# Kernel tuning notes

Measured on AMD Instinct MI355X. Metric: run time of the kernel, lower is better.

## Reference

```python
import jax, jax.numpy as jnp
import numpy as np

D_MODEL = 512
NUM_HEADS = 8
WINDOW = 10
DEPTH = D_MODEL // NUM_HEADS


def positional_encoding(position, d_model):
    pos = np.arange(position)[:, None].astype(np.float32)
    i = np.arange(d_model)[None, :].astype(np.float32)
    angle = pos / np.power(10000.0, 2.0 * (np.floor(i / 2.0)) / np.float32(d_model))
    angle[:, 0::2] = np.sin(angle[:, 0::2])
    angle[:, 1::2] = np.cos(angle[:, 1::2])
    return jnp.asarray(angle[None, ...], dtype=jnp.float32)  # [1, n, d_model]


def forward(x, wq_w, wq_b, wk_w, wk_b, wv_w, wv_b, dense_w, dense_b):
    B, C, S, _ = x.shape
    data = x[..., 0]
    mask = x[..., 2]
    data = data.reshape(B, C, -1, WINDOW)   # [B,C,n,W]
    mask = mask.reshape(B, C, -1, WINDOW)
    n = data.shape[2]

    # mean_module: (data*mask).mean over window, drop first/last window
    mean_feature = jnp.mean(data * mask, axis=-1, keepdims=True)[:, :, 1:-1]  # [B,C,n-2,1]

    # combined look-ahead + padding mask
    mask_min = jnp.min(mask[:, :, 1:-1], axis=-1)              # [B,C,n-2]
    n2 = n - 2
    look_ahead = 1.0 - jnp.tril(jnp.ones((n2, n2), jnp.float32))
    padding = (mask_min == 0).astype(jnp.float32)[:, :, None, None, :]  # [B,C,1,1,n-2]
    comb_mask = jnp.maximum(look_ahead, padding)               # [B,C,1,n-2,n-2]

    # positional encoding over window dimension
    pe = positional_encoding(n, WINDOW)                        # [1,n,W]
    data = data + pe[None]                                     # [B,C,n,W]

    # q,k from concatenated future/past windows; v from current windows
    qk_in = jnp.concatenate([data[:, :, 2:], data[:, :, :-2]], axis=-1)  # [B,C,n-2,2W]
    q = qk_in @ wq_w + wq_b
    k = qk_in @ wk_w + wk_b
    v = data[:, :, 1:-1] @ wv_w + wv_b                          # [B,C,n-2,d_model]

    def split_heads(t):
        return t.reshape(B, C, n2, NUM_HEADS, DEPTH).transpose(0, 1, 3, 2, 4)

    q, k, v = split_heads(q), split_heads(k), split_heads(v)    # [B,C,H,n-2,depth]

    logits = jnp.einsum('bchqd,bchkd->bchqk', q, k) / jnp.sqrt(jnp.float32(DEPTH))
    logits = logits + comb_mask * (-1e9)
    attn = jax.nn.softmax(logits, axis=-1)
    ctx = jnp.einsum('bchqk,bchkd->bchqd', attn, v)
    ctx = ctx.transpose(0, 1, 3, 2, 4).reshape(B, C, n2, D_MODEL)

    concat = jnp.concatenate([ctx, mean_feature], axis=-1)      # [B,C,n-2,d_model+1]
    out = concat @ dense_w + dense_b                            # [B,C,n-2,W]
    return out.reshape(B, C, -1)[..., None]                     # [B,C,(n-2)*W,1]


def setup_inputs() -> dict:
    key = jax.random.key(0)
    ks = jax.random.split(key, 8)
    B, C, S = 16, 16, 2560
    data = jax.random.normal(ks[0], (B, C, S), jnp.float32)
    time = jnp.zeros((B, C, S), jnp.float32)
    mask = (jax.random.uniform(ks[1], (B, C, S)) < 0.9).astype(jnp.float32)
    x = jnp.stack([data, time, mask], axis=-1)
    scale = 0.02
    return {
        'x': x,
        'wq_w': jax.random.normal(ks[2], (2 * WINDOW, D_MODEL), jnp.float32) * scale,
        'wq_b': jnp.zeros((D_MODEL,), jnp.float32),
        'wk_w': jax.random.normal(ks[3], (2 * WINDOW, D_MODEL), jnp.float32) * scale,
        'wk_b': jnp.zeros((D_MODEL,), jnp.float32),
        'wv_w': jax.random.normal(ks[4], (WINDOW, D_MODEL), jnp.float32) * scale,
        'wv_b': jnp.zeros((D_MODEL,), jnp.float32),
        'dense_w': jax.random.normal(ks[5], (D_MODEL + 1, WINDOW), jnp.float32) * scale,
        'dense_b': jnp.zeros((WINDOW,), jnp.float32),
    }


def reference(x, wq_w, wq_b, wk_w, wk_b, wv_w, wv_b, dense_w, dense_b):
    return forward(x, wq_w, wq_b, wk_w, wk_b, wv_w, wv_b, dense_w, dense_b)
```

## Files before the change

kernel.cpp:

```cpp
#include <hip/hip_runtime.h>

#define LOG2E 1.44269504088896340736f

typedef __bf16 bf16x8 __attribute__((ext_vector_type(8)));
typedef float f32x16 __attribute__((ext_vector_type(16)));

union U4B { uint4 u; bf16x8 v; };

static __device__ __forceinline__ unsigned short f2bf(float f) {
  unsigned u = __builtin_bit_cast(unsigned, f);
  u += 0x7FFFu + ((u >> 16) & 1u);
  return (unsigned short)(u >> 16);
}
static __device__ __forceinline__ float bf2f(unsigned short s) {
  unsigned u = ((unsigned)s) << 16;
  return __builtin_bit_cast(float, u);
}
static __device__ __forceinline__ f32x16 zero16() {
  f32x16 z;
#pragma unroll
  for (int i = 0; i < 16; ++i) z[i] = 0.f;
  return z;
}
static __device__ __forceinline__ f32x16 MFMA(bf16x8 a, bf16x8 b, f32x16 c) {
  return __builtin_amdgcn_mfma_f32_32x32x16_bf16(a, b, c, 0, 0, 0);
}

static __device__ __forceinline__ void xform(f32x16 t, int hi, uint4& f0, uint4& f1) {
  unsigned pk[8], sw[8];
#pragma unroll
  for (int s = 0; s < 8; ++s) {
    unsigned d;
    asm("v_cvt_pk_bf16_f32 %0, %1, %2" : "=v"(d) : "v"(t[2*s]), "v"(t[2*s+1]));
    pk[s] = d;
  }
#pragma unroll
  for (int s = 0; s < 8; ++s) sw[s] = (unsigned)__shfl_xor((int)pk[s], 32);
  if (hi) {
    f0 = make_uint4(sw[2], sw[3], pk[2], pk[3]);
    f1 = make_uint4(sw[6], sw[7], pk[6], pk[7]);
  } else {
    f0 = make_uint4(pk[0], pk[1], sw[0], sw[1]);
    f1 = make_uint4(pk[4], pk[5], sw[4], sw[5]);
  }
}

__global__ void zero_out_k(float* __restrict__ out, int n) {
  int i = blockIdx.x * 256 + threadIdx.x;
  if (i < n) out[i] = 0.f;
}

__global__ void setup_k(
    const float* __restrict__ wq_w, const float* __restrict__ wq_b,
    const float* __restrict__ wk_w, const float* __restrict__ wk_b,
    const float* __restrict__ wv_w, const float* __restrict__ wv_b,
    const float* __restrict__ dense_w, float* __restrict__ ws)
{
  int gid = blockIdx.x*256 + threadIdx.x;
  float* pe = ws;
  unsigned short* wqT = (unsigned short*)(ws + 2560);
  unsigned short* wkT = (unsigned short*)(ws + 10752);
  float* WVD = ws + 18944;
  float* bvd = ws + 19744;
  if (gid < 2560) {
    int i = gid/10, t = gid%10;
    double ex = (double)(2*(t/2)) / 10.0;
    double ang = (double)i * pow(10000.0, -ex);
    pe[gid] = (float)((t & 1) ? cos(ang) : sin(ang));
  } else if (gid < 2560 + 16384) {
    int idx = gid - 2560;
    int hd = idx >> 5, t = idx & 31;
    float v = (t < 20) ? wq_w[t*512 + hd] : ((t == 20) ? wq_b[hd] : 0.f);
    wqT[idx] = f2bf(v);
  } else if (gid < 2560 + 32768) {
    int idx = gid - (2560 + 16384);
    int hd = idx >> 5, t = idx & 31;
    float v = (t < 20) ? wk_w[t*512 + hd] : ((t == 20) ? wk_b[hd] : 0.f);
    wkT[idx] = f2bf(v);
  } else if (gid < 2560 + 32768 + 800) {
    int idx = gid - (2560 + 32768);
    int h = idx/100, rem = idx%100, t = rem/10, w = rem%10;
    float s = 0.f;
    for (int d = 0; d < 64; ++d) s += wv_w[t*512 + h*64 + d] * dense_w[(h*64 + d)*10 + w];
    WVD[idx] = s;
  } else if (gid < 2560 + 32768 + 880) {
    int idx = gid - (2560 + 32768 + 800);
    int h = idx/10, w = idx%10;
    float s = 0.f;
    for (int d = 0; d < 64; ++d) s += wv_b[h*64 + d] * dense_w[(h*64 + d)*10 + w];
    bvd[idx] = s;
  }
}

__global__ __launch_bounds__(256, 1) void mha_fused(
    const float* __restrict__ x,
    const float* __restrict__ dense_w, const float* __restrict__ dense_b,
    const unsigned short* __restrict__ wqT, const unsigned short* __restrict__ wkT,
    const float* __restrict__ WVD, const float* __restrict__ bvd,
    const float* __restrict__ pe,
    float* __restrict__ out)
{
  __shared__ __align__(16) unsigned short qk_in[256*24];
  __shared__ __align__(16) unsigned short k_lds[256*64];
  __shared__ __align__(16) unsigned short vdT[32*256];
  __shared__ float mean_l[256];
  __shared__ unsigned long long padb[4];
  __shared__ float part[160];
  __shared__ float ddmean_s[10];

  const int tid = threadIdx.x;
  const int lane = tid & 63;
  const int wv = tid >> 6;
  const int hi = lane >> 5;
  const int cc = lane & 31;
  const int bc = blockIdx.x >> 1;
  const int parity = blockIdx.x & 1;

  float ddr[10];
  {
    const float* xb = x + ((size_t)bc*2560 + tid*10)*3;
    float dat[10], msk[10];
#pragma unroll
    for (int t = 0; t < 10; ++t) { dat[t] = xb[3*t]; msk[t] = xb[3*t+2]; }
    float mean = 0.f, mm = msk[0];
#pragma unroll
    for (int t = 0; t < 10; ++t) { mean += dat[t]*msk[t]; mm = fminf(mm, msk[t]); }
    mean_l[tid] = mean * 0.1f;
    const float* per = pe + tid*10;
#pragma unroll
    for (int t = 0; t < 10; ++t) ddr[t] = dat[t] + per[t];
    float* ddtmp = (float*)k_lds;
    float* mmv = ddtmp + 2560;
#pragma unroll
    for (int t = 0; t < 10; ++t) ddtmp[tid*10 + t] = ddr[t];
    mmv[tid] = mm;
  }
  __syncthreads();
  {
    const float* ddtmp = (const float*)k_lds;
    const float* mmv = ddtmp + 2560;
    if (tid < 254) {
#pragma unroll
      for (int t = 0; t < 10; ++t) qk_in[tid*24 + t] = f2bf(ddtmp[(tid+2)*10 + t]);
#pragma unroll
      for (int t = 0; t < 10; ++t) qk_in[tid*24 + 10 + t] = f2bf(ddr[t]);
      qk_in[tid*24 + 20] = 0x3F80;
      qk_in[tid*24 + 21] = 0; qk_in[tid*24 + 22] = 0; qk_in[tid*24 + 23] = 0;
    } else {
#pragma unroll
      for (int t = 0; t < 24; ++t) qk_in[tid*24 + t] = 0;
    }
    if (tid < 160) {
      int t = tid >> 4, j = tid & 15;
      int w0 = 1 + j*16, w1 = (w0 + 16 < 255) ? (w0 + 16) : 255;
      float s = 0.f;
      for (int w = w0; w < w1; ++w) s += ddtmp[w*10 + t];
      part[tid] = s;
    }
    bool cond = (tid < 254) && (mmv[tid+1] == 0.0f);
    unsigned long long bl = __ballot(cond);
    if (lane == 0) padb[wv] = bl;
  }
  __syncthreads();
  if (tid < 10) {
    float s = 0.f;
#pragma unroll
    for (int j = 0; j < 16; ++j) s += part[tid*16 + j];
    ddmean_s[tid] = s * (1.0f/254.0f);
  }
  float dwcol = 0.f, dbias = 0.f;
  if (cc < 10) { dwcol = dense_w[5120 + cc]; dbias = dense_b[cc]; }
  const unsigned* pw = (const unsigned*)padb;

  f32x16 outacc0 = zero16(), outacc1 = zero16();

#pragma unroll 1
  for (int hh = 0; hh < 4; ++hh) {
    const int h = parity*4 + hh;
    __syncthreads();
    if (tid < 254) {
      float df[10];
      int src = tid + 1;
      if (src <= 253) {
#pragma unroll
        for (int t = 0; t < 10; ++t) df[t] = bf2f(qk_in[src*24 + 10 + t]);
      } else {
#pragma unroll
        for (int t = 0; t < 10; ++t) df[t] = bf2f(qk_in[252*24 + t]);
      }
      const float* wvd = WVD + h*100;
      const float* bv = bvd + h*10;
#pragma unroll
      for (int w = 0; w < 10; ++w) {
        float s = bv[w];
#pragma unroll
        for (int t = 0; t < 10; ++t) s += df[t]*wvd[t*10 + w];
        vdT[w*256 + (tid ^ ((w & 15)*8))] = f2bf(s);
      }
    }
    if (tid < 64) {
      int w = tid >> 1, j = 254 + (tid & 1);
      vdT[w*256 + (j ^ ((w & 15)*8))] = 0;
    }
    float mvd = 0.f;
    if (cc < 10) {
      mvd = bvd[h*10 + cc];
#pragma unroll
      for (int t = 0; t < 10; ++t) mvd = fmaf(ddmean_s[t], WVD[h*100 + t*10 + cc], mvd);
    }
    __syncthreads();

#pragma unroll
    for (int jti = 0; jti < 2; ++jti) {
      int jt = wv + 4*jti;
      int krow = 32*jt + cc;
      U4B b0, b1;
      b0.u = *(const uint4*)&qk_in[krow*24 + 8*hi];
      b1.u = make_uint4(0,0,0,0);
      if (!hi) b1.u = *(const uint4*)&qk_in[krow*24 + 16];
#pragma unroll
      for (int it = 0; it < 2; ++it) {
        const unsigned short* wrow = wkT + (h*64 + 32*it + cc)*32;
        U4B a0, a1;
        a0.u = *(const uint4*)&wrow[8*hi];
        a1.u = *(const uint4*)&wrow[16 + 8*hi];
        f32x16 acc = zero16();
        acc = MFMA(a0.v, b0.v, acc);
        acc = MFMA(a1.v, b1.v, acc);
        uint4 f0, f1;
        xform(acc, hi, f0, f1);
        int dc0 = 2*it, dc1 = 2*it + 1;
        *(uint4*)&k_lds[krow*64 + ((8*(2*dc0 + hi)) ^ (8*(krow & 7)))] = f0;
        *(uint4*)&k_lds[krow*64 + ((8*(2*dc1 + hi)) ^ (8*(krow & 7)))] = f1;
      }
    }
    __syncthreads();

#pragma unroll
    for (int qti = 0; qti < 2; ++qti) {
      const int qt = qti ? (7 - wv) : wv;
      const int qrow = 32*qt + cc;
      uint4 qf0, qf1, qf2, qf3;
      {
        U4B b0, b1;
        b0.u = *(const uint4*)&qk_in[qrow*24 + 8*hi];
        b1.u = make_uint4(0,0,0,0);
        if (!hi) b1.u = *(const uint4*)&qk_in[qrow*24 + 16];
        {
          const unsigned short* wrow = wqT + (h*64 + cc)*32;
          U4B a0, a1;
          a0.u = *(const uint4*)&wrow[8*hi];
          a1.u = *(const uint4*)&wrow[16 + 8*hi];
          f32x16 acc = zero16();
          acc = MFMA(a0.v, b0.v, acc);
          acc = MFMA(a1.v, b1.v, acc);
          xform(acc, hi, qf0, qf1);
        }
        {
          const unsigned short* wrow = wqT + (h*64 + 32 + cc)*32;
          U4B a0, a1;
          a0.u = *(const uint4*)&wrow[8*hi];
          a1.u = *(const uint4*)&wrow[16 + 8*hi];
          f32x16 acc = zero16();
          acc = MFMA(a0.v, b0.v, acc);
          acc = MFMA(a1.v, b1.v, acc);
          xform(acc, hi, qf2, qf3);
        }
      }
      f32x16 st[8];
#pragma unroll
      for (int kt = 0; kt < 8; ++kt) {
        if (kt <= qt) {
          const int kr = 32*kt + cc;
          const int kbase = kr*64;
          const int ksw = 8*(kr & 7);
          f32x16 a = zero16();
          U4B ka, qa;
          ka.u = *(const uint4*)&k_lds[kbase + ((8*(0 + hi)) ^ ksw)];
          qa.u = qf0; a = MFMA(ka.v, qa.v, a);
          ka.u = *(const uint4*)&k_lds[kbase + ((8*(2 + hi)) ^ ksw)];
          qa.u = qf1; a = MFMA(ka.v, qa.v, a);
          ka.u = *(const uint4*)&k_lds[kbase + ((8*(4 + hi)) ^ ksw)];
          qa.u = qf2; a = MFMA(ka.v, qa.v, a);
          ka.u = *(const uint4*)&k_lds[kbase + ((8*(6 + hi)) ^ ksw)];
          qa.u = qf3; a = MFMA(ka.v, qa.v, a);
          const unsigned pbk = pw[kt];
#pragma unroll
          for (int r = 0; r < 16; ++r) {
            const int base = (r & 3) + 8*(r >> 2);
            const int key = 32*kt + base + 4*hi;
            bool mk = (key > qrow) || (((pbk >> (base + 4*hi)) & 1u) != 0u);
            float mv = mk ? -1e9f : 0.f;
            if (kt == 7 && r >= 14) mv = hi ? -1e30f : mv;
            a[r] = a[r]*0.125f + mv;
          }
          st[kt] = a;
        }
      }
      float m = st[0][0];
#pragma unroll
      for (int kt = 0; kt < 8; ++kt) {
        if (kt <= qt) {
#pragma unroll
          for (int r = 0; r < 16; ++r) m = fmaxf(m, st[kt][r]);
        }
      }
      m = fmaxf(m, __shfl_xor(m, 32));
      const float mL = m * LOG2E;
      float sum = 0.f;
#pragma unroll
      for (int kt = 0; kt < 8; ++kt) {
        if (kt <= qt) {
          float sk = 0.f;
#pragma unroll
          for (int r = 0; r < 16; ++r) {
            float p = exp2f(fmaf(st[kt][r], LOG2E, -mL));
            st[kt][r] = p;
            sk += p;
          }
          sum += sk;
        }
      }
      sum += __shfl_xor(sum, 32);
      const float rs = 1.0f / sum;
      f32x16 pv = zero16();
#pragma unroll
      for (int kt = 0; kt < 8; ++kt) {
        if (kt <= qt) {
          uint4 pa0, pa1;
          xform(st[kt], hi, pa0, pa1);
          U4B pA, vB;
          pA.u = pa0;
          vB.u = *(const uint4*)&vdT[cc*256 + ((32*kt + 8*hi) ^ (8*(cc & 15)))];
          pv = MFMA(pA.v, vB.v, pv);
          pA.u = pa1;
          vB.u = *(const uint4*)&vdT[cc*256 + ((32*kt + 16 + 8*hi) ^ (8*(cc & 15)))];
          pv = MFMA(pA.v, vB.v, pv);
        }
      }
      bool pre = true;
#pragma unroll
      for (int j = 0; j < 8; ++j) { if (j < qt) pre = pre && (pw[j] == 0xFFFFFFFFu); }
      const unsigned pbq = pw[qt];
#pragma unroll
      for (int r = 0; r < 16; ++r) {
        const int base = (r & 3) + 8*(r >> 2);
        const int qr = base + 4*hi;
        unsigned lm = (qr == 31) ? 0xFFFFFFFFu : ((2u << qr) - 1u);
        bool degq = pre && ((pbq & lm) == lm);
        float rr = __shfl(rs, qr, 32);
        float contrib = degq ? mvd : pv[r]*rr;
        if (qti == 0) outacc0[r] += contrib; else outacc1[r] += contrib;
      }
    }
  }

#pragma unroll
  for (int qti = 0; qti < 2; ++qti) {
    const int qt = qti ? (7 - wv) : wv;
#pragma unroll
    for (int r = 0; r < 16; ++r) {
      const int base = (r & 3) + 8*(r >> 2);
      int q = 32*qt + base + 4*hi;
      if (q < 254 && cc < 10) {
        float v = (qti == 0 ? outacc0[r] : outacc1[r]);
        if (parity == 0) v += mean_l[q + 1]*dwcol + dbias;
        atomicAdd(&out[((size_t)bc*254 + q)*10 + cc], v);
      }
    }
  }
}

extern "C" void kernel_launch(void* const* d_in, const int* in_sizes, int n_in,
                              void* d_out, int out_size, void* d_ws, size_t ws_size,
                              hipStream_t stream) {
  const float* x       = (const float*)d_in[0];
  const float* wq_w    = (const float*)d_in[1];
  const float* wq_b    = (const float*)d_in[2];
  const float* wk_w    = (const float*)d_in[3];
  const float* wk_b    = (const float*)d_in[4];
  const float* wv_w    = (const float*)d_in[5];
  const float* wv_b    = (const float*)d_in[6];
  const float* dense_w = (const float*)d_in[7];
  const float* dense_b = (const float*)d_in[8];
  float* ws = (float*)d_ws;

  zero_out_k<<<(out_size + 255)/256, 256, 0, stream>>>((float*)d_out, out_size);
  setup_k<<<142, 256, 0, stream>>>(wq_w, wq_b, wk_w, wk_b, wv_w, wv_b, dense_w, ws);
  mha_fused<<<512, 256, 0, stream>>>(
      x, dense_w, dense_b,
      (const unsigned short*)(ws + 2560),
      (const unsigned short*)(ws + 10752),
      ws + 18944,
      ws + 19744,
      ws,
      (float*)d_out);
}
```

Baseline: 220.5 us.

## Drop softmax max pass, fuse exp with PV, split heads across three blocks

Removes the separate row-max reduction and stored score tiles. It computes exp2 directly with a folded scale constant and large negative mask offsets, then feeds each tile into the PV MFMA immediately. The grid goes from 512 to 768 blocks, each handling 3/3/2 heads. Shared memory is shrunk (half-size vdT, bf16 mean, part aliased into vdT) so more blocks can be resident. Skipping max subtraction risks overflow for large logits and adds more atomic adds per output.

```diff
diff --git a/kernel.cpp b/kernel.cpp
--- a/kernel.cpp
+++ b/kernel.cpp
@@ -1,6 +1,7 @@
 #include <hip/hip_runtime.h>
 
 #define LOG2E 1.44269504088896340736f
+#define SCL 0.18033688011111772f
 
 typedef __bf16 bf16x8 __attribute__((ext_vector_type(8)));
 typedef float f32x16 __attribute__((ext_vector_type(16)));
@@ -102,10 +103,9 @@
 {
   __shared__ __align__(16) unsigned short qk_in[256*24];
   __shared__ __align__(16) unsigned short k_lds[256*64];
-  __shared__ __align__(16) unsigned short vdT[32*256];
-  __shared__ float mean_l[256];
+  __shared__ __align__(16) unsigned short vdT[16*256];
+  __shared__ unsigned short mean_b[256];
   __shared__ unsigned long long padb[4];
-  __shared__ float part[160];
   __shared__ float ddmean_s[10];
 
   const int tid = threadIdx.x;
@@ -113,8 +113,10 @@
   const int wv = tid >> 6;
   const int hi = lane >> 5;
   const int cc = lane & 31;
-  const int bc = blockIdx.x >> 1;
-  const int parity = blockIdx.x & 1;
+  const int bc = blockIdx.x / 3;
+  const int p3 = blockIdx.x - bc*3;
+  const int hbase = p3*3;
+  const int nh = (p3 == 2) ? 2 : 3;
 
   float ddr[10];
   {
@@ -125,7 +127,7 @@
     float mean = 0.f, mm = msk[0];
 #pragma unroll
     for (int t = 0; t < 10; ++t) { mean += dat[t]*msk[t]; mm = fminf(mm, msk[t]); }
-    mean_l[tid] = mean * 0.1f;
+    mean_b[tid] = f2bf(mean * 0.1f);
     const float* per = pe + tid*10;
 #pragma unroll
     for (int t = 0; t < 10; ++t) ddr[t] = dat[t] + per[t];
@@ -139,6 +141,7 @@
   {
     const float* ddtmp = (const float*)k_lds;
     const float* mmv = ddtmp + 2560;
+    float* part = (float*)vdT;
     if (tid < 254) {
 #pragma unroll
       for (int t = 0; t < 10; ++t) qk_in[tid*24 + t] = f2bf(ddtmp[(tid+2)*10 + t]);
@@ -157,12 +160,15 @@
       for (int w = w0; w < w1; ++w) s += ddtmp[w*10 + t];
       part[tid] = s;
     }
-    bool cond = (tid < 254) && (mmv[tid+1] == 0.0f);
+#pragma unroll
+    for (int i = 0; i < 6; ++i) vdT[(10 + i)*256 + tid] = 0;
+    bool cond = (tid >= 254) || (mmv[tid+1] == 0.0f);
     unsigned long long bl = __ballot(cond);
     if (lane == 0) padb[wv] = bl;
   }
   __syncthreads();
   if (tid < 10) {
+    const float* part = (const float*)vdT;
     float s = 0.f;
 #pragma unroll
     for (int j = 0; j < 16; ++j) s += part[tid*16 + j];
@@ -175,8 +181,8 @@
   f32x16 outacc0 = zero16(), outacc1 = zero16();
 
 #pragma unroll 1
-  for (int hh = 0; hh < 4; ++hh) {
-    const int h = parity*4 + hh;
+  for (int hh = 0; hh < nh; ++hh) {
+    const int h = hbase + hh;
     __syncthreads();
     if (tid < 254) {
       float df[10];
@@ -198,7 +204,7 @@
         vdT[w*256 + (tid ^ ((w & 15)*8))] = f2bf(s);
       }
     }
-    if (tid < 64) {
+    if (tid < 32) {
       int w = tid >> 1, j = 254 + (tid & 1);
       vdT[w*256 + (j ^ ((w & 15)*8))] = 0;
     }
@@ -267,7 +273,10 @@
           xform(acc, hi, qf2, qf3);
         }
       }
-      f32x16 st[8];
+      float sum = 0.f;
+      f32x16 pv = zero16();
+      const int vrow = cc & 15;
+      const int vsw = 8*vrow;
 #pragma unroll
       for (int kt = 0; kt < 8; ++kt) {
         if (kt <= qt) {
@@ -285,59 +294,41 @@
           ka.u = *(const uint4*)&k_lds[kbase + ((8*(6 + hi)) ^ ksw)];
           qa.u = qf3; a = MFMA(ka.v, qa.v, a);
           const unsigned pbk = pw[kt];
-#pragma unroll
-          for (int r = 0; r < 16; ++r) {
-            const int base = (r & 3) + 8*(r >> 2);
-            const int key = 32*kt + base + 4*hi;
-            bool mk = (key > qrow) || (((pbk >> (base + 4*hi)) & 1u) != 0u);
-            float mv = mk ? -1e9f : 0.f;
-            if (kt == 7 && r >= 14) mv = hi ? -1e30f : mv;
-            a[r] = a[r]*0.125f + mv;
+          if (kt < qt) {
+#pragma unroll
+            for (int r = 0; r < 16; ++r) {
+              const int base = (r & 3) + 8*(r >> 2);
+              const int pos = base + 4*hi;
+              float add = ((pbk >> pos) & 1u) ? -2.0e9f : 0.0f;
+              float p = exp2f(fmaf(a[r], SCL, add));
+              a[r] = p;
+              sum += p;
+            }
+          } else {
+#pragma unroll
+            for (int r = 0; r < 16; ++r) {
+              const int base = (r & 3) + 8*(r >> 2);
+              const int pos = base + 4*hi;
+              bool mk = (((pbk >> pos) & 1u) != 0u) || (pos > cc);
+              float add = mk ? -2.0e9f : 0.0f;
+              float p = exp2f(fmaf(a[r], SCL, add));
+              a[r] = p;
+              sum += p;
+            }
           }
-          st[kt] = a;
-        }
-      }
-      float m = st[0][0];
-#pragma unroll
-      for (int kt = 0; kt < 8; ++kt) {
-        if (kt <= qt) {
-#pragma unroll
-          for (int r = 0; r < 16; ++r) m = fmaxf(m, st[kt][r]);
-        }
-      }
-      m = fmaxf(m, __shfl_xor(m, 32));
-      const float mL = m * LOG2E;
-      float sum = 0.f;
-#pragma unroll
-      for (int kt = 0; kt < 8; ++kt) {
-        if (kt <= qt) {
-          float sk = 0.f;
-#pragma unroll
-          for (int r = 0; r < 16; ++r) {
-            float p = exp2f(fmaf(st[kt][r], LOG2E, -mL));
-            st[kt][r] = p;
-            sk += p;
-          }
-          sum += sk;
-        }
-      }
-      sum += __shfl_xor(sum, 32);
-      const float rs = 1.0f / sum;
-      f32x16 pv = zero16();
-#pragma unroll
-      for (int kt = 0; kt < 8; ++kt) {
-        if (kt <= qt) {
           uint4 pa0, pa1;
-          xform(st[kt], hi, pa0, pa1);
+          xform(a, hi, pa0, pa1);
           U4B pA, vB;
           pA.u = pa0;
-          vB.u = *(const uint4*)&vdT[cc*256 + ((32*kt + 8*hi) ^ (8*(cc & 15)))];
+          vB.u = *(const uint4*)&vdT[vrow*256 + ((32*kt + 8*hi) ^ vsw)];
           pv = MFMA(pA.v, vB.v, pv);
           pA.u = pa1;
-          vB.u = *(const uint4*)&vdT[cc*256 + ((32*kt + 16 + 8*hi) ^ (8*(cc & 15)))];
+          vB.u = *(const uint4*)&vdT[vrow*256 + ((32*kt + 16 + 8*hi) ^ vsw)];
           pv = MFMA(pA.v, vB.v, pv);
         }
       }
+      float stot = sum + __shfl_xor(sum, 32);
+      const float rs = 1.0f / fmaxf(stot, 1e-30f);
       bool pre = true;
 #pragma unroll
       for (int j = 0; j < 8; ++j) { if (j < qt) pre = pre && (pw[j] == 0xFFFFFFFFu); }
@@ -364,7 +355,7 @@
       int q = 32*qt + base + 4*hi;
       if (q < 254 && cc < 10) {
         float v = (qti == 0 ? outacc0[r] : outacc1[r]);
-        if (parity == 0) v += mean_l[q + 1]*dwcol + dbias;
+        if (p3 == 0) v += bf2f(mean_b[q + 1])*dwcol + dbias;
         atomicAdd(&out[((size_t)bc*254 + q)*10 + cc], v);
       }
     }
@@ -387,7 +378,7 @@
 
   zero_out_k<<<(out_size + 255)/256, 256, 0, stream>>>((float*)d_out, out_size);
   setup_k<<<142, 256, 0, stream>>>(wq_w, wq_b, wk_w, wk_b, wv_w, wv_b, dense_w, ws);
-  mha_fused<<<512, 256, 0, stream>>>(
+  mha_fused<<<768, 256, 0, stream>>>(
       x, dense_w, dense_b,
       (const unsigned short*)(ws + 2560),
       (const unsigned short*)(ws + 10752),
```

After: 201.7 us. 8.5% less time.
